# Optimization experiments

Measured on AMD Instinct MI355X. Metric: run time of the kernel, lower is better.

The kernel has to match this reference:

```python
import jax, jax.numpy as jnp
import numpy as np

DIM = 1024
HEADS = 16
DIM_HEAD = 64
INNER = HEADS * DIM_HEAD  # 1024


def setup_inputs() -> dict:
    key = jax.random.key(0)
    ks = jax.random.split(key, 5)
    B, N = 4, 2048
    x = jax.random.normal(ks[0], (B, N, DIM), dtype=jnp.float32)
    # nn.Linear weights stored as [out, in]; we keep [in, out] for x @ W
    s = 1.0 / np.sqrt(DIM)
    Wq = jax.random.uniform(ks[1], (DIM, INNER), jnp.float32, -s, s)
    Wkv = jax.random.uniform(ks[2], (DIM, 2 * INNER), jnp.float32, -s, s)
    so = 1.0 / np.sqrt(INNER)
    Wo = jax.random.uniform(ks[3], (INNER, DIM), jnp.float32, -so, so)
    bo = jax.random.uniform(ks[4], (DIM,), jnp.float32, -so, so)
    return {"x": x, "Wq": Wq, "Wkv": Wkv, "Wo": Wo, "bo": bo}


def reference(x, Wq, Wkv, Wo, bo):
    B, N, _ = x.shape
    scale = DIM_HEAD ** -0.5
    q = x @ Wq                      # [B, N, INNER]
    kv = x @ Wkv                    # [B, N, 2*INNER]
    k, v = jnp.split(kv, 2, axis=-1)

    def split_heads(t):
        return t.reshape(B, N, HEADS, DIM_HEAD).transpose(0, 2, 1, 3)  # b h n d

    q, k, v = map(split_heads, (q, k, v))
    dots = jnp.einsum('bhid,bhjd->bhij', q, k) * scale
    # causal mask: positions j > i filled with -inf
    causal = jnp.triu(jnp.ones((N, N), dtype=bool), k=1)
    dots = jnp.where(causal, -jnp.inf, dots)
    attn = jax.nn.softmax(dots, axis=-1)
    out = jnp.einsum('bhij,bhjd->bhid', attn, v)
    out = out.transpose(0, 2, 1, 3).reshape(B, N, INNER)
    return out @ Wo + bo
```

## Files before the change

kernel.cpp:

```cpp
#include <hip/hip_runtime.h>
#include <hip/hip_bf16.h>
#include <math.h>

typedef __attribute__((ext_vector_type(8))) short bf16x8;
typedef __attribute__((ext_vector_type(4))) float f32x4;

static __device__ inline ushort f2bf(float f) {
    union { float f; unsigned u; } v; v.f = f;
    unsigned r = (v.u + 0x7fff + ((v.u >> 16) & 1)) >> 16;
    return (ushort)r;
}

#define GLD_LDS(g, l) \
    __builtin_amdgcn_global_load_lds( \
        (const __attribute__((address_space(1))) void*)(g), \
        (__attribute__((address_space(3))) void*)(l), 16, 0, 0)

__global__ __launch_bounds__(256) void convert_x(
    const float* __restrict__ x, ushort* __restrict__ xb)
{
    const size_t i = ((size_t)blockIdx.x * 256 + threadIdx.x) * 8;
    float4 a = *(const float4*)(x + i);
    float4 b = *(const float4*)(x + i + 4);
    bf16x8 t;
    t[0] = (short)f2bf(a.x); t[1] = (short)f2bf(a.y);
    t[2] = (short)f2bf(a.z); t[3] = (short)f2bf(a.w);
    t[4] = (short)f2bf(b.x); t[5] = (short)f2bf(b.y);
    t[6] = (short)f2bf(b.z); t[7] = (short)f2bf(b.w);
    *(bf16x8*)(xb + i) = t;
}

__global__ __launch_bounds__(256) void prep_w(
    const float* __restrict__ Wq, const float* __restrict__ Wkv,
    const float* __restrict__ Wo, ushort* __restrict__ Wt)
{
    const int w = threadIdx.x >> 6;
    const int lane = threadIdx.x & 63;
    const int tile = blockIdx.x * 4 + w;
    const int r0 = (tile >> 4) << 6;
    const int k0 = (tile & 15) << 6;

    const float* src; int ld, c0;
    if (r0 < 1024)      { src = Wq;  ld = 1024; c0 = r0; }
    else if (r0 < 3072) { src = Wkv; ld = 2048; c0 = r0 - 1024; }
    else                { src = Wo;  ld = 1024; c0 = r0 - 3072; }

    ushort v[64];
    #pragma unroll
    for (int k = 0; k < 64; ++k)
        v[k] = f2bf(src[(size_t)(k0 + k) * ld + c0 + lane]);

    ushort* dst = Wt + (size_t)(r0 + lane) * 1024 + k0;
    #pragma unroll
    for (int k = 0; k < 64; k += 8) {
        bf16x8 t;
        #pragma unroll
        for (int j = 0; j < 8; ++j) t[j] = (short)v[k + j];
        *(bf16x8*)(dst + k) = t;
    }
}

#define STG32(t, Ad, Bd) { \
    GLD_LDS(aS + (size_t)(t) * 32, (Ad) + ldst); \
    GLD_LDS(bSlo + (size_t)(t) * 32, (Bd) + ldst); \
    GLD_LDS(bShi + (size_t)(t) * 32, (Bd) + 128 * 32 + ldst); }

#define GEMM_PIPE(Aptr, Btptr, NXT, NWG)                                       \
    __shared__ ushort As[3][128 * 32];                                         \
    __shared__ ushort Bs[3][256 * 32];                                         \
    const int tid = threadIdx.x;                                               \
    const int lane = tid & 63;                                                 \
    const int w = tid >> 6;                                                    \
    const int l15 = lane & 15;                                                 \
    const int quad = lane >> 4;                                                \
    const int wm = w >> 2, wn = w & 3;                                         \
    const int lin = blockIdx.y * (NXT) + blockIdx.x;                           \
    const int wg = (lin & 7) * ((NWG) >> 3) + (lin >> 3);                      \
    const int rowBase = (wg / (NXT)) * 128;                                    \
    const int colBase = (wg % (NXT)) * 256;                                    \
                         \
    const int sr = tid >> 2, sc = tid & 3;                                     \
    const int ldst = sr * 32 + sc * 8;                                         \
    const int gsw = (sc ^ ((sr >> 1) & 3)) << 3;                               \
    const ushort* aS   = (Aptr)  + (size_t)(rowBase + sr) * 1024 + gsw;        \
    const ushort* bSlo = (Btptr) + (size_t)(colBase + sr) * 1024 + gsw;        \
    const ushort* bShi = bSlo + (size_t)128 * 1024;                            \
    \
    const int co = ((quad ^ ((l15 >> 1) & 3)) << 3);                           \
    f32x4 acc[4][4];                                                           \
    _Pragma("unroll")                                                          \
    for (int i_ = 0; i_ < 4; ++i_)                                             \
        _Pragma("unroll")                                                      \
        for (int j_ = 0; j_ < 4; ++j_) acc[i_][j_] = (f32x4){0.f, 0.f, 0.f, 0.f}; \
    ushort *Acur = As[0], *Anxt = As[1], *Apre = As[2];                        \
    ushort *Bcur = Bs[0], *Bnxt = Bs[1], *Bpre = Bs[2];                        \
    STG32(0, Acur, Bcur)                                                       \
    STG32(1, Anxt, Bnxt)                                                       \
    asm volatile("s_waitcnt vmcnt(3)" ::: "memory");                           \
    __builtin_amdgcn_s_barrier();                                              \
    asm volatile("" ::: "memory");                                             \
    _Pragma("unroll 1")                                                        \
    for (int u = 0; u < 32; ++u) {                                             \
        if (u + 2 < 32) { STG32(u + 2, Apre, Bpre) }                           \
        const ushort* aC = Acur + (wm * 64 + l15) * 32;                        \
        const ushort* bC = Bcur + (wn * 64 + l15) * 32;                        \
        bf16x8 aF[4], bF[4];                                                   \
        _Pragma("unroll")                                                      \
        for (int ni = 0; ni < 4; ++ni)                                         \
            bF[ni] = *(const bf16x8*)(bC + ni * 512 + co);                     \
        _Pragma("unroll")                                                      \
        for (int mi = 0; mi < 4; ++mi)                                         \
            aF[mi] = *(const bf16x8*)(aC + mi * 512 + co);                     \
        __builtin_amdgcn_s_setprio(1);                                         \
        _Pragma("unroll")                                                      \
        for (int mi = 0; mi < 4; ++mi)                                         \
            _Pragma("unroll")                                                  \
            for (int ni = 0; ni < 4; ++ni)                                     \
                acc[mi][ni] = __builtin_amdgcn_mfma_f32_16x16x32_bf16(         \
                    aF[mi], bF[ni], acc[mi][ni], 0, 0, 0);                     \
        __builtin_amdgcn_s_setprio(0);                                         \
        if (u < 30)       { asm volatile("s_waitcnt vmcnt(3)" ::: "memory"); } \
        else if (u == 30) { asm volatile("s_waitcnt vmcnt(0)" ::: "memory"); } \
        if (u < 31) {                                                          \
            __builtin_amdgcn_s_barrier();                                      \
            asm volatile("" ::: "memory");                                     \
        }                                                                      \
        ushort* tA = Acur; Acur = Anxt; Anxt = Apre; Apre = tA;                \
        ushort* tB = Bcur; Bcur = Bnxt; Bnxt = Bpre; Bpre = tB;                \
    }

__global__ __launch_bounds__(512, 4) void gemm_qkv(
    const ushort* __restrict__ A, const ushort* __restrict__ Bt,
    ushort* __restrict__ Qb, ushort* __restrict__ Kb, ushort* __restrict__ Vt)
{
    GEMM_PIPE(A, Bt, 12, 768)

    const int seg = colBase >> 10;
    if (seg == 2) {
        #pragma unroll
        for (int mi = 0; mi < 4; ++mi) {
            #pragma unroll
            for (int ni = 0; ni < 4; ++ni) {
                const int c = (colBase + wn*64 + ni*16 + l15) & 1023;
                const int h = c >> 6, d = c & 63;
                const int m = rowBase + wm*64 + mi*16 + quad*4;
                const int b = m >> 11, nn = m & 2047;
                ushort4 v;
                v.x = f2bf(acc[mi][ni][0]); v.y = f2bf(acc[mi][ni][1]);
                v.z = f2bf(acc[mi][ni][2]); v.w = f2bf(acc[mi][ni][3]);
                *(ushort4*)(Vt + ((size_t)(b*16 + h)*64 + d)*2048 + nn) = v;
            }
        }
    } else {
        ushort* dst = seg ? Kb : Qb;
        const float sc2 = seg ? 1.0f : 0.18033688011112042f;
        #pragma unroll
        for (int mi = 0; mi < 4; ++mi) {
            #pragma unroll
            for (int ni = 0; ni < 4; ++ni) {
                const int c = (colBase + wn*64 + ni*16 + l15) & 1023;
                const int h = c >> 6, d = c & 63;
                #pragma unroll
                for (int r = 0; r < 4; ++r) {
                    const int m = rowBase + wm*64 + mi*16 + quad*4 + r;
                    const int b = m >> 11, nn = m & 2047;
                    dst[((((size_t)b*16 + h)*2048 + nn) << 6) + d] = f2bf(acc[mi][ni][r] * sc2);
                }
            }
        }
    }
}

__global__ __launch_bounds__(512, 4) void gemm_out(
    const ushort* __restrict__ A, const ushort* __restrict__ Bt,
    const float* __restrict__ bo, float* __restrict__ out)
{
    GEMM_PIPE(A, Bt, 4, 256)

    #pragma unroll
    for (int mi = 0; mi < 4; ++mi) {
        #pragma unroll
        for (int ni = 0; ni < 4; ++ni) {
            const int n = colBase + wn*64 + ni*16 + l15;
            const float bb = bo[n];
            #pragma unroll
            for (int r = 0; r < 4; ++r) {
                const int m = rowBase + wm*64 + mi*16 + quad*4 + r;
                out[(size_t)m * 1024 + n] = acc[mi][ni][r] + bb;
            }
        }
    }
}

__device__ __forceinline__ bf16x8 lds_frag(const ushort* S, int row, int chunk) {
    return *(const bf16x8*)(S + row * 64 + ((chunk ^ (row & 7)) << 3));
}

__global__ __launch_bounds__(256, 2) void flash_mfma(
    const ushort* __restrict__ Qb,
    const ushort* __restrict__ Kb,
    const ushort* __restrict__ Vt,
    ushort* __restrict__ Ob)
{
    __shared__ ushort Ks[2][4096];
    __shared__ ushort Vs[2][4096];
    __shared__ ushort PsAll[4][32][72];

    const int tid = threadIdx.x;
    const int w = tid >> 6;
    const int lane = tid & 63;
    const int l15 = lane & 15;
    const int quad = lane >> 4;
    ushort (*Ps)[72] = PsAll[w];

    const int blk = blockIdx.x;
    const int bh = ((blk & 7) << 3) | ((blk >> 3) & 7);
    const int qt = 15 - (blk >> 6);
    const int nt = 2 * qt + 2;
    const int rb0 = (qt << 7) + w * 32;

    const int sr0 = tid >> 3, sr1 = sr0 + 32;
    const int cg0 = (tid & 7) ^ (sr0 & 7);
    const int cg1 = (tid & 7) ^ (sr1 & 7);
    const ushort* kgb = Kb + (size_t)bh * 131072;
    const ushort* vgb = Vt + (size_t)bh * 131072;

    bf16x8 qf[2][2];
    #pragma unroll
    for (int mi = 0; mi < 2; ++mi) {
        const ushort* qp = Qb + ((size_t)bh * 2048 + rb0 + mi*16 + l15) * 64 + quad * 8;
        qf[mi][0] = *(const bf16x8*)qp;
        qf[mi][1] = *(const bf16x8*)(qp + 32);
    }

    bf16x8 bones;
    #pragma unroll
    for (int j = 0; j < 8; ++j) bones[j] = (short)0x3F80;

    float m_r[2];
    f32x4 o[2][4], lacc[2];
    #pragma unroll
    for (int mi = 0; mi < 2; ++mi) {
        m_r[mi] = -INFINITY;
        lacc[mi] = (f32x4){0.f, 0.f, 0.f, 0.f};
        #pragma unroll
        for (int nb = 0; nb < 4; ++nb) o[mi][nb] = (f32x4){0.f, 0.f, 0.f, 0.f};
    }

    GLD_LDS(kgb + sr0*64 + cg0*8, &Ks[0][tid*8]);
    GLD_LDS(kgb + sr1*64 + cg1*8, &Ks[0][tid*8 + 2048]);
    GLD_LDS(vgb + (size_t)sr0*2048 + cg0*8, &Vs[0][tid*8]);
    GLD_LDS(vgb + (size_t)sr1*2048 + cg1*8, &Vs[0][tid*8 + 2048]);

    for (int t = 0; t < nt; ++t) {
        __syncthreads();
        const int cur = t & 1;
        if (t + 1 < nt) {
            const int jn = t + 1;
            ushort* kd = &Ks[cur ^ 1][tid * 8];
            ushort* vd = &Vs[cur ^ 1][tid * 8];
            GLD_LDS(kgb + (size_t)jn*4096 + sr0*64 + cg0*8, kd);
            GLD_LDS(kgb + (size_t)jn*4096 + sr1*64 + cg1*8, kd + 2048);
            GLD_LDS(vgb + (size_t)sr0*2048 + jn*64 + cg0*8, vd);
            GLD_LDS(vgb + (size_t)sr1*2048 + jn*64 + cg1*8, vd + 2048);
        }
        const int j0 = t << 6;
        if (j0 > rb0 + 31) continue;

        const ushort* Ksb = Ks[cur];
        const ushort* Vsb = Vs[cur];

        f32x4 St[2][4];
        #pragma unroll
        for (int kb = 0; kb < 4; ++kb) {
            bf16x8 ka = lds_frag(Ksb, kb*16 + l15, quad);
            bf16x8 kc = lds_frag(Ksb, kb*16 + l15, quad + 4);
            #pragma unroll
            for (int mi = 0; mi < 2; ++mi) {
                f32x4 s = (f32x4){0.f, 0.f, 0.f, 0.f};
                s = __builtin_amdgcn_mfma_f32_16x16x32_bf16(ka, qf[mi][0], s, 0, 0, 0);
                s = __builtin_amdgcn_mfma_f32_16x16x32_bf16(kc, qf[mi][1], s, 0, 0, 0);
                St[mi][kb] = s;
            }
        }

        #pragma unroll
        for (int mi = 0; mi < 2; ++mi) {
            const int qrow = rb0 + mi*16 + l15;
            if (j0 + 63 > rb0 + mi*16) {
                #pragma unroll
                for (int kb = 0; kb < 4; ++kb) {
                    const int kbase = j0 + kb*16 + quad*4;
                    #pragma unroll
                    for (int r = 0; r < 4; ++r)
                        if (kbase + r > qrow) St[mi][kb][r] = -INFINITY;
                }
            }
            f32x4 mv = St[mi][0];
            #pragma unroll
            for (int kb = 1; kb < 4; ++kb)
                #pragma unroll
                for (int r = 0; r < 4; ++r) mv[r] = fmaxf(mv[r], St[mi][kb][r]);
            float mx = fmaxf(fmaxf(mv[0], mv[1]), fmaxf(mv[2], mv[3]));
            mx = fmaxf(mx, __shfl_xor(mx, 16));
            mx = fmaxf(mx, __shfl_xor(mx, 32));
            const float mold = m_r[mi];
            const float mnew = fmaxf(mold, mx);
            if (__any(mnew > mold)) {
                m_r[mi] = mnew;
                const float corr = __builtin_amdgcn_exp2f(mold - mnew);
                float ct[4];
                #pragma unroll
                for (int r = 0; r < 4; ++r) ct[r] = __shfl(corr, quad*4 + r);
                #pragma unroll
                for (int r = 0; r < 4; ++r) lacc[mi][r] *= ct[r];
                #pragma unroll
                for (int nb = 0; nb < 4; ++nb)
                    #pragma unroll
                    for (int r = 0; r < 4; ++r) o[mi][nb][r] *= ct[r];
            }
            #pragma unroll
            for (int kb = 0; kb < 4; ++kb)
                #pragma unroll
                for (int r = 0; r < 4; ++r)
                    St[mi][kb][r] = __builtin_amdgcn_exp2f(St[mi][kb][r] - mnew);
            #pragma unroll
            for (int kb = 0; kb < 4; ++kb) {
                union { float f; unsigned u; } c0, c1, c2, c3;
                c0.f = St[mi][kb][0]; c1.f = St[mi][kb][1];
                c2.f = St[mi][kb][2]; c3.f = St[mi][kb][3];
                uint2 pk;
                pk.x = (c0.u >> 16) | (c1.u & 0xFFFF0000u);
                pk.y = (c2.u >> 16) | (c3.u & 0xFFFF0000u);
                *(uint2*)&Ps[mi*16 + l15][kb*16 + quad*4] = pk;
            }
        }

        bf16x8 pf[2][2];
        #pragma unroll
        for (int mi = 0; mi < 2; ++mi) {
            pf[mi][0] = *(const bf16x8*)&Ps[mi*16 + l15][quad * 8];
            pf[mi][1] = *(const bf16x8*)&Ps[mi*16 + l15][32 + quad * 8];
        }
        #pragma unroll
        for (int mi = 0; mi < 2; ++mi) {
            lacc[mi] = __builtin_amdgcn_mfma_f32_16x16x32_bf16(pf[mi][0], bones, lacc[mi], 0, 0, 0);
            lacc[mi] = __builtin_amdgcn_mfma_f32_16x16x32_bf16(pf[mi][1], bones, lacc[mi], 0, 0, 0);
        }
        #pragma unroll
        for (int nb = 0; nb < 4; ++nb) {
            bf16x8 va = lds_frag(Vsb, nb*16 + l15, quad);
            bf16x8 vc = lds_frag(Vsb, nb*16 + l15, quad + 4);
            #pragma unroll
            for (int mi = 0; mi < 2; ++mi) {
                o[mi][nb] = __builtin_amdgcn_mfma_f32_16x16x32_bf16(pf[mi][0], va, o[mi][nb], 0, 0, 0);
                o[mi][nb] = __builtin_amdgcn_mfma_f32_16x16x32_bf16(pf[mi][1], vc, o[mi][nb], 0, 0, 0);
            }
        }
    }

    const int b = bh >> 4, h = bh & 15;
    #pragma unroll
    for (int mi = 0; mi < 2; ++mi)
        #pragma unroll
        for (int r = 0; r < 4; ++r) {
            const int ig = rb0 + mi*16 + quad*4 + r;
            const float inv = 1.f / lacc[mi][r];
            ushort* op = Ob + ((size_t)(b * 2048 + ig)) * 1024 + h * 64 + l15;
            #pragma unroll
            for (int nb = 0; nb < 4; ++nb)
                op[nb * 16] = f2bf(o[mi][nb][r] * inv);
        }
}

extern "C" void kernel_launch(void* const* d_in, const int* in_sizes, int n_in,
                              void* d_out, int out_size, void* d_ws, size_t ws_size,
                              hipStream_t stream) {
    const float* x   = (const float*)d_in[0];
    const float* Wq  = (const float*)d_in[1];
    const float* Wkv = (const float*)d_in[2];
    const float* Wo  = (const float*)d_in[3];
    const float* bo  = (const float*)d_in[4];
    float* out = (float*)d_out;

    const size_t SEG = (size_t)8388608 * 2;
    char* ws = (char*)d_ws;
    ushort* xb = (ushort*)(ws);
    ushort* Qb = (ushort*)(ws + SEG);
    ushort* Kb = (ushort*)(ws + SEG * 2);
    ushort* Vt = (ushort*)(ws + SEG * 3);
    ushort* Ob = (ushort*)(ws + SEG * 4);
    ushort* Wt = (ushort*)(ws + SEG * 5);

    convert_x<<<dim3(4096), 256, 0, stream>>>(x, xb);
    prep_w<<<dim3(256), 256, 0, stream>>>(Wq, Wkv, Wo, Wt);
    gemm_qkv<<<dim3(12, 64), 512, 0, stream>>>(xb, Wt, Qb, Kb, Vt);
    flash_mfma<<<dim3(1024), 256, 0, stream>>>(Qb, Kb, Vt, Ob);
    gemm_out<<<dim3(4, 64), 512, 0, stream>>>(Ob, Wt + (size_t)3072 * 1024, bo, out);
}
```

Measured before the change: 259.1 us.

## Rewrite QKV GEMM with 256x256 tiles and K=64 double-buffered staged pipeline

```diff
diff --git a/kernel.cpp b/kernel.cpp
--- a/kernel.cpp
+++ b/kernel.cpp
@@ -15,6 +15,8 @@
     __builtin_amdgcn_global_load_lds( \
         (const __attribute__((address_space(1))) void*)(g), \
         (__attribute__((address_space(3))) void*)(l), 16, 0, 0)
+
+#define MFMA_BF16(a, b, c) __builtin_amdgcn_mfma_f32_16x16x32_bf16((a), (b), (c), 0, 0, 0)
 
 __global__ __launch_bounds__(256) void convert_x(
     const float* __restrict__ x, ushort* __restrict__ xb)
@@ -57,6 +59,200 @@
         #pragma unroll
         for (int j = 0; j < 8; ++j) t[j] = (short)v[k + j];
         *(bf16x8*)(dst + k) = t;
+    }
+}
+
+#define STG_A256(t, h) { \
+    ushort* d_ = As2 + ((t) & 1) * 16384 + (h) * 8192 + tid * 8; \
+    GLD_LDS(aG + (size_t)((h) * 128) * 1024 + (size_t)(t) * 64, d_); \
+    GLD_LDS(aG + (size_t)((h) * 128 + 64) * 1024 + (size_t)(t) * 64, d_ + 4096); }
+#define STG_B256(t, h) { \
+    ushort* d_ = Bs2 + ((t) & 1) * 16384 + (h) * 8192 + tid * 8; \
+    GLD_LDS(bG + (size_t)((h) * 128) * 1024 + (size_t)(t) * 64, d_); \
+    GLD_LDS(bG + (size_t)((h) * 128 + 64) * 1024 + (size_t)(t) * 64, d_ + 4096); }
+
+__global__ __launch_bounds__(512, 2) void gemm_qkv(
+    const ushort* __restrict__ A, const ushort* __restrict__ Bt,
+    ushort* __restrict__ Qb, ushort* __restrict__ Kb, ushort* __restrict__ Vt)
+{
+    __shared__ ushort As2[2 * 2 * 8192];
+    __shared__ ushort Bs2[2 * 2 * 8192];
+
+    const int tid = threadIdx.x;
+    const int lane = tid & 63;
+    const int w = tid >> 6;
+    const int l15 = lane & 15;
+    const int quad = lane >> 4;
+    const int wm = w >> 2, wn = w & 3;
+
+    const int lin = blockIdx.y * 12 + blockIdx.x;
+    const int wg = (lin & 7) * 48 + (lin >> 3);
+    const int rowBase = (wg / 12) * 256;
+    const int colBase = (wg % 12) * 256;
+
+    const int srow = tid >> 3;
+    const int gsw = ((tid & 7) ^ (srow & 7)) << 3;
+    const ushort* aG = A  + (size_t)(rowBase + srow) * 1024 + gsw;
+    const ushort* bG = Bt + (size_t)(colBase + srow) * 1024 + gsw;
+
+    const int c0 = (quad ^ (l15 & 7)) << 3;
+    const int c1 = c0 ^ 32;
+
+    f32x4 acc[8][4];
+    #pragma unroll
+    for (int i_ = 0; i_ < 8; ++i_)
+        #pragma unroll
+        for (int j_ = 0; j_ < 4; ++j_) acc[i_][j_] = (f32x4){0.f, 0.f, 0.f, 0.f};
+
+    STG_A256(0, 0) STG_A256(0, 1) STG_B256(0, 0) STG_B256(0, 1)
+    asm volatile("s_waitcnt vmcnt(4)" ::: "memory");
+    STG_B256(1, 0) STG_A256(1, 0) STG_A256(1, 1)
+    asm volatile("s_waitcnt vmcnt(6)" ::: "memory");
+    __builtin_amdgcn_s_barrier();
+    asm volatile("" ::: "memory");
+
+    #pragma unroll 1
+    for (int t = 0; t < 16; ++t) {
+        const int cur = t & 1;
+        const ushort* Ar = As2 + cur * 16384;
+        const ushort* Br = Bs2 + cur * 16384;
+        const ushort* a0p = Ar + (wm * 64 + l15) * 64;
+        const ushort* a1p = a0p + 8192;
+        const ushort* bp  = Br + (wn >> 1) * 8192 + ((wn & 1) * 64 + l15) * 64;
+
+        bf16x8 b0[4], b1[4];
+        #pragma unroll
+        for (int ni = 0; ni < 4; ++ni) {
+            b0[ni] = *(const bf16x8*)(bp + ni * 1024 + c0);
+            b1[ni] = *(const bf16x8*)(bp + ni * 1024 + c1);
+        }
+        bf16x8 aE0 = *(const bf16x8*)(a0p + c0);
+        bf16x8 aO0 = *(const bf16x8*)(a0p + c1);
+        bf16x8 aE1 = *(const bf16x8*)(a0p + 1024 + c0);
+        bf16x8 aO1 = *(const bf16x8*)(a0p + 1024 + c1);
+        if (t + 1 < 16) { STG_B256(t + 1, 1) }
+        __builtin_amdgcn_s_barrier();
+        asm volatile("s_waitcnt lgkmcnt(0)" ::: "memory");
+        __builtin_amdgcn_sched_barrier(0);
+        __builtin_amdgcn_s_setprio(1);
+        #pragma unroll
+        for (int ni = 0; ni < 4; ++ni) {
+            acc[0][ni] = MFMA_BF16(aE0, b0[ni], acc[0][ni]);
+            acc[0][ni] = MFMA_BF16(aO0, b1[ni], acc[0][ni]);
+        }
+        #pragma unroll
+        for (int ni = 0; ni < 4; ++ni) {
+            acc[1][ni] = MFMA_BF16(aE1, b0[ni], acc[1][ni]);
+            acc[1][ni] = MFMA_BF16(aO1, b1[ni], acc[1][ni]);
+        }
+        __builtin_amdgcn_s_setprio(0);
+        __builtin_amdgcn_s_barrier();
+        asm volatile("" ::: "memory");
+
+        bf16x8 aE2 = *(const bf16x8*)(a0p + 2048 + c0);
+        bf16x8 aO2 = *(const bf16x8*)(a0p + 2048 + c1);
+        bf16x8 aE3 = *(const bf16x8*)(a0p + 3072 + c0);
+        bf16x8 aO3 = *(const bf16x8*)(a0p + 3072 + c1);
+        if (t + 2 < 16) { STG_B256(t + 2, 0) }
+        __builtin_amdgcn_s_barrier();
+        asm volatile("s_waitcnt lgkmcnt(0)" ::: "memory");
+        __builtin_amdgcn_sched_barrier(0);
+        __builtin_amdgcn_s_setprio(1);
+        #pragma unroll
+        for (int ni = 0; ni < 4; ++ni) {
+            acc[2][ni] = MFMA_BF16(aE2, b0[ni], acc[2][ni]);
+            acc[2][ni] = MFMA_BF16(aO2, b1[ni], acc[2][ni]);
+        }
+        #pragma unroll
+        for (int ni = 0; ni < 4; ++ni) {
+            acc[3][ni] = MFMA_BF16(aE3, b0[ni], acc[3][ni]);
+            acc[3][ni] = MFMA_BF16(aO3, b1[ni], acc[3][ni]);
+        }
+        __builtin_amdgcn_s_setprio(0);
+        __builtin_amdgcn_s_barrier();
+        asm volatile("" ::: "memory");
+
+        bf16x8 s1E[4], s1O[4];
+        #pragma unroll
+        for (int rf = 0; rf < 4; ++rf) {
+            s1E[rf] = *(const bf16x8*)(a1p + rf * 1024 + c0);
+            s1O[rf] = *(const bf16x8*)(a1p + rf * 1024 + c1);
+        }
+        if (t + 2 < 16) { STG_A256(t + 2, 0) }
+        __builtin_amdgcn_s_barrier();
+        asm volatile("s_waitcnt lgkmcnt(0)" ::: "memory");
+        __builtin_amdgcn_sched_barrier(0);
+        __builtin_amdgcn_s_setprio(1);
+        #pragma unroll
+        for (int ni = 0; ni < 4; ++ni) {
+            acc[4][ni] = MFMA_BF16(s1E[0], b0[ni], acc[4][ni]);
+            acc[4][ni] = MFMA_BF16(s1O[0], b1[ni], acc[4][ni]);
+        }
+        #pragma unroll
+        for (int ni = 0; ni < 4; ++ni) {
+            acc[5][ni] = MFMA_BF16(s1E[1], b0[ni], acc[5][ni]);
+            acc[5][ni] = MFMA_BF16(s1O[1], b1[ni], acc[5][ni]);
+        }
+        __builtin_amdgcn_s_setprio(0);
+        __builtin_amdgcn_s_barrier();
+        asm volatile("" ::: "memory");
+
+        if (t + 2 < 16) { STG_A256(t + 2, 1) }
+        __builtin_amdgcn_s_barrier();
+        __builtin_amdgcn_sched_barrier(0);
+        __builtin_amdgcn_s_setprio(1);
+        #pragma unroll
+        for (int ni = 0; ni < 4; ++ni) {
+            acc[6][ni] = MFMA_BF16(s1E[2], b0[ni], acc[6][ni]);
+            acc[6][ni] = MFMA_BF16(s1O[2], b1[ni], acc[6][ni]);
+        }
+        #pragma unroll
+        for (int ni = 0; ni < 4; ++ni) {
+            acc[7][ni] = MFMA_BF16(s1E[3], b0[ni], acc[7][ni]);
+            acc[7][ni] = MFMA_BF16(s1O[3], b1[ni], acc[7][ni]);
+        }
+        __builtin_amdgcn_s_setprio(0);
+        if (t < 14)       { asm volatile("s_waitcnt vmcnt(6)" ::: "memory"); }
+        else if (t == 14) { asm volatile("s_waitcnt vmcnt(0)" ::: "memory"); }
+        if (t < 15) {
+            __builtin_amdgcn_s_barrier();
+            asm volatile("" ::: "memory");
+        }
+    }
+
+    const int seg = colBase >> 10;
+    if (seg == 2) {
+        #pragma unroll
+        for (int ri = 0; ri < 8; ++ri) {
+            #pragma unroll
+            for (int ni = 0; ni < 4; ++ni) {
+                const int c = (colBase + wn*64 + ni*16 + l15) & 1023;
+                const int h = c >> 6, d = c & 63;
+                const int m = rowBase + ((ri >> 2) << 7) + wm*64 + (ri & 3)*16 + quad*4;
+                const int b = m >> 11, nn = m & 2047;
+                ushort4 v;
+                v.x = f2bf(acc[ri][ni][0]); v.y = f2bf(acc[ri][ni][1]);
+                v.z = f2bf(acc[ri][ni][2]); v.w = f2bf(acc[ri][ni][3]);
+                *(ushort4*)(Vt + ((size_t)(b*16 + h)*64 + d)*2048 + nn) = v;
+            }
+        }
+    } else {
+        ushort* dst = seg ? Kb : Qb;
+        const float sc2 = seg ? 1.0f : 0.18033688011112042f;
+        #pragma unroll
+        for (int ri = 0; ri < 8; ++ri) {
+            #pragma unroll
+            for (int ni = 0; ni < 4; ++ni) {
+                const int c = (colBase + wn*64 + ni*16 + l15) & 1023;
+                const int h = c >> 6, d = c & 63;
+                #pragma unroll
+                for (int r = 0; r < 4; ++r) {
+                    const int m = rowBase + ((ri >> 2) << 7) + wm*64 + (ri & 3)*16 + quad*4 + r;
+                    const int b = m >> 11, nn = m & 2047;
+                    dst[((((size_t)b*16 + h)*2048 + nn) << 6) + d] = f2bf(acc[ri][ni][r] * sc2);
+                }
+            }
+        }
     }
 }
 
@@ -78,14 +274,12 @@
     const int wg = (lin & 7) * ((NWG) >> 3) + (lin >> 3);                      \
     const int rowBase = (wg / (NXT)) * 128;                                    \
     const int colBase = (wg % (NXT)) * 256;                                    \
-                         \
     const int sr = tid >> 2, sc = tid & 3;                                     \
     const int ldst = sr * 32 + sc * 8;                                         \
     const int gsw = (sc ^ ((sr >> 1) & 3)) << 3;                               \
     const ushort* aS   = (Aptr)  + (size_t)(rowBase + sr) * 1024 + gsw;        \
     const ushort* bSlo = (Btptr) + (size_t)(colBase + sr) * 1024 + gsw;        \
     const ushort* bShi = bSlo + (size_t)128 * 1024;                            \
-    \
     const int co = ((quad ^ ((l15 >> 1) & 3)) << 3);                           \
     f32x4 acc[4][4];                                                           \
     _Pragma("unroll")                                                          \
@@ -129,48 +323,6 @@
         ushort* tB = Bcur; Bcur = Bnxt; Bnxt = Bpre; Bpre = tB;                \
     }
 
-__global__ __launch_bounds__(512, 4) void gemm_qkv(
-    const ushort* __restrict__ A, const ushort* __restrict__ Bt,
-    ushort* __restrict__ Qb, ushort* __restrict__ Kb, ushort* __restrict__ Vt)
-{
-    GEMM_PIPE(A, Bt, 12, 768)
-
-    const int seg = colBase >> 10;
-    if (seg == 2) {
-        #pragma unroll
-        for (int mi = 0; mi < 4; ++mi) {
-            #pragma unroll
-            for (int ni = 0; ni < 4; ++ni) {
-                const int c = (colBase + wn*64 + ni*16 + l15) & 1023;
-                const int h = c >> 6, d = c & 63;
-                const int m = rowBase + wm*64 + mi*16 + quad*4;
-                const int b = m >> 11, nn = m & 2047;
-                ushort4 v;
-                v.x = f2bf(acc[mi][ni][0]); v.y = f2bf(acc[mi][ni][1]);
-                v.z = f2bf(acc[mi][ni][2]); v.w = f2bf(acc[mi][ni][3]);
-                *(ushort4*)(Vt + ((size_t)(b*16 + h)*64 + d)*2048 + nn) = v;
-            }
-        }
-    } else {
-        ushort* dst = seg ? Kb : Qb;
-        const float sc2 = seg ? 1.0f : 0.18033688011112042f;
-        #pragma unroll
-        for (int mi = 0; mi < 4; ++mi) {
-            #pragma unroll
-            for (int ni = 0; ni < 4; ++ni) {
-                const int c = (colBase + wn*64 + ni*16 + l15) & 1023;
-                const int h = c >> 6, d = c & 63;
-                #pragma unroll
-                for (int r = 0; r < 4; ++r) {
-                    const int m = rowBase + wm*64 + mi*16 + quad*4 + r;
-                    const int b = m >> 11, nn = m & 2047;
-                    dst[((((size_t)b*16 + h)*2048 + nn) << 6) + d] = f2bf(acc[mi][ni][r] * sc2);
-                }
-            }
-        }
-    }
-}
-
 __global__ __launch_bounds__(512, 4) void gemm_out(
     const ushort* __restrict__ A, const ushort* __restrict__ Bt,
     const float* __restrict__ bo, float* __restrict__ out)
@@ -278,8 +430,8 @@
             #pragma unroll
             for (int mi = 0; mi < 2; ++mi) {
                 f32x4 s = (f32x4){0.f, 0.f, 0.f, 0.f};
-                s = __builtin_amdgcn_mfma_f32_16x16x32_bf16(ka, qf[mi][0], s, 0, 0, 0);
-                s = __builtin_amdgcn_mfma_f32_16x16x32_bf16(kc, qf[mi][1], s, 0, 0, 0);
+                s = MFMA_BF16(ka, qf[mi][0], s);
+                s = MFMA_BF16(kc, qf[mi][1], s);
                 St[mi][kb] = s;
             }
         }
@@ -326,12 +478,12 @@
                     St[mi][kb][r] = __builtin_amdgcn_exp2f(St[mi][kb][r] - mnew);
             #pragma unroll
             for (int kb = 0; kb < 4; ++kb) {
-                union { float f; unsigned u; } c0, c1, c2, c3;
-                c0.f = St[mi][kb][0]; c1.f = St[mi][kb][1];
-                c2.f = St[mi][kb][2]; c3.f = St[mi][kb][3];
+                union { float f; unsigned u; } c0_, c1_, c2_, c3_;
+                c0_.f = St[mi][kb][0]; c1_.f = St[mi][kb][1];
+                c2_.f = St[mi][kb][2]; c3_.f = St[mi][kb][3];
                 uint2 pk;
-                pk.x = (c0.u >> 16) | (c1.u & 0xFFFF0000u);
-                pk.y = (c2.u >> 16) | (c3.u & 0xFFFF0000u);
+                pk.x = (c0_.u >> 16) | (c1_.u & 0xFFFF0000u);
+                pk.y = (c2_.u >> 16) | (c3_.u & 0xFFFF0000u);
                 *(uint2*)&Ps[mi*16 + l15][kb*16 + quad*4] = pk;
             }
         }
@@ -344,8 +496,8 @@
         }
         #pragma unroll
         for (int mi = 0; mi < 2; ++mi) {
-            lacc[mi] = __builtin_amdgcn_mfma_f32_16x16x32_bf16(pf[mi][0], bones, lacc[mi], 0, 0, 0);
-            lacc[mi] = __builtin_amdgcn_mfma_f32_16x16x32_bf16(pf[mi][1], bones, lacc[mi], 0, 0, 0);
+            lacc[mi] = MFMA_BF16(pf[mi][0], bones, lacc[mi]);
+            lacc[mi] = MFMA_BF16(pf[mi][1], bones, lacc[mi]);
         }
         #pragma unroll
         for (int nb = 0; nb < 4; ++nb) {
@@ -353,8 +505,8 @@
             bf16x8 vc = lds_frag(Vsb, nb*16 + l15, quad + 4);
             #pragma unroll
             for (int mi = 0; mi < 2; ++mi) {
-                o[mi][nb] = __builtin_amdgcn_mfma_f32_16x16x32_bf16(pf[mi][0], va, o[mi][nb], 0, 0, 0);
-                o[mi][nb] = __builtin_amdgcn_mfma_f32_16x16x32_bf16(pf[mi][1], vc, o[mi][nb], 0, 0, 0);
+                o[mi][nb] = MFMA_BF16(pf[mi][0], va, o[mi][nb]);
+                o[mi][nb] = MFMA_BF16(pf[mi][1], vc, o[mi][nb]);
             }
         }
     }
@@ -394,7 +546,7 @@
 
     convert_x<<<dim3(4096), 256, 0, stream>>>(x, xb);
     prep_w<<<dim3(256), 256, 0, stream>>>(Wq, Wkv, Wo, Wt);
-    gemm_qkv<<<dim3(12, 64), 512, 0, stream>>>(xb, Wt, Qb, Kb, Vt);
+    gemm_qkv<<<dim3(12, 32), 512, 0, stream>>>(xb, Wt, Qb, Kb, Vt);
     flash_mfma<<<dim3(1024), 256, 0, stream>>>(Qb, Kb, Vt, Ob);
     gemm_out<<<dim3(4, 64), 512, 0, stream>>>(Ob, Wt + (size_t)3072 * 1024, bo, out);
 }
```

Result: no change. 258.1 us (-0.4%).

## Enlarge QKV GEMM tiles to 256x384 with double-buffered LDS staging

Applied to the files above, without the earlier changes.

```diff
diff --git a/kernel.cpp b/kernel.cpp
--- a/kernel.cpp
+++ b/kernel.cpp
@@ -15,6 +15,8 @@
     __builtin_amdgcn_global_load_lds( \
         (const __attribute__((address_space(1))) void*)(g), \
         (__attribute__((address_space(3))) void*)(l), 16, 0, 0)
+
+#define MFMA_BF16(a, b, c) __builtin_amdgcn_mfma_f32_16x16x32_bf16((a), (b), (c), 0, 0, 0)
 
 __global__ __launch_bounds__(256) void convert_x(
     const float* __restrict__ x, ushort* __restrict__ xb)
@@ -57,6 +59,109 @@
         #pragma unroll
         for (int j = 0; j < 8; ++j) t[j] = (short)v[k + j];
         *(bf16x8*)(dst + k) = t;
+    }
+}
+
+#define STG_A96(t) { ushort* d_ = As2 + ((t) & 1) * 8192 + ldst; \
+    GLD_LDS(aG + (size_t)(t) * 32, d_); \
+    GLD_LDS(aG + (size_t)131072 + (size_t)(t) * 32, d_ + 4096); }
+#define STG_B96(t) { ushort* d_ = Bs2 + ((t) & 1) * 12288 + ldst; \
+    GLD_LDS(bG + (size_t)(t) * 32, d_); \
+    GLD_LDS(bG + (size_t)131072 + (size_t)(t) * 32, d_ + 4096); \
+    GLD_LDS(bG + (size_t)262144 + (size_t)(t) * 32, d_ + 8192); }
+
+__global__ __launch_bounds__(512, 2) void gemm_qkv(
+    const ushort* __restrict__ A, const ushort* __restrict__ Bt,
+    ushort* __restrict__ Qb, ushort* __restrict__ Kb, ushort* __restrict__ Vt)
+{
+    __shared__ ushort As2[2 * 8192];
+    __shared__ ushort Bs2[2 * 12288];
+
+    const int tid = threadIdx.x;
+    const int lane = tid & 63;
+    const int w = tid >> 6;
+    const int l15 = lane & 15;
+    const int quad = lane >> 4;
+    const int wm = w >> 2, wn = w & 3;
+
+    const int lin = blockIdx.y * 8 + blockIdx.x;
+    const int wg = (lin & 7) * 32 + (lin >> 3);
+    const int rowBase = (wg >> 3) * 256;
+    const int colBase = (wg & 7) * 384;
+
+    const int sr = tid >> 2, sc = tid & 3;
+    const int ldst = sr * 32 + sc * 8;
+    const int gsw = (sc ^ ((sr >> 1) & 3)) << 3;
+    const ushort* aG = A  + (size_t)(rowBase + sr) * 1024 + gsw;
+    const ushort* bG = Bt + (size_t)(colBase + sr) * 1024 + gsw;
+
+    const int co = (quad ^ ((l15 >> 1) & 3)) << 3;
+
+    f32x4 acc[8][6];
+    #pragma unroll
+    for (int i_ = 0; i_ < 8; ++i_)
+        #pragma unroll
+        for (int j_ = 0; j_ < 6; ++j_) acc[i_][j_] = (f32x4){0.f, 0.f, 0.f, 0.f};
+
+    STG_A96(0) STG_B96(0)
+    asm volatile("s_waitcnt vmcnt(0)" ::: "memory");
+    __builtin_amdgcn_s_barrier();
+    asm volatile("" ::: "memory");
+
+    #pragma unroll 1
+    for (int t = 0; t < 32; ++t) {
+        const int cur = t & 1;
+        if (t + 1 < 32) { STG_A96(t + 1) STG_B96(t + 1) }
+
+        const ushort* aRd = As2 + cur * 8192  + (wm * 128 + l15) * 32;
+        const ushort* bRd = Bs2 + cur * 12288 + (wn * 96 + l15) * 32;
+
+        bf16x8 bF[6];
+        #pragma unroll
+        for (int ni = 0; ni < 6; ++ni)
+            bF[ni] = *(const bf16x8*)(bRd + ni * 512 + co);
+
+        __builtin_amdgcn_s_setprio(1);
+        #pragma unroll
+        for (int ri = 0; ri < 8; ++ri) {
+            bf16x8 aF = *(const bf16x8*)(aRd + ri * 512 + co);
+            #pragma unroll
+            for (int ni = 0; ni < 6; ++ni)
+                acc[ri][ni] = MFMA_BF16(aF, bF[ni], acc[ri][ni]);
+        }
+        __builtin_amdgcn_s_setprio(0);
+
+        asm volatile("s_waitcnt vmcnt(0)" ::: "memory");
+        __builtin_amdgcn_s_barrier();
+        asm volatile("" ::: "memory");
+    }
+
+    const float qsc = 0.18033688011112042f;
+    #pragma unroll
+    for (int ri = 0; ri < 8; ++ri) {
+        #pragma unroll
+        for (int ni = 0; ni < 6; ++ni) {
+            const int c = colBase + wn * 96 + ni * 16 + l15;
+            const int seg = c >> 10;
+            const int h = (c & 1023) >> 6, d = c & 63;
+            if (seg == 2) {
+                const int m = rowBase + wm * 128 + ri * 16 + quad * 4;
+                const int b = m >> 11, nn = m & 2047;
+                ushort4 v;
+                v.x = f2bf(acc[ri][ni][0]); v.y = f2bf(acc[ri][ni][1]);
+                v.z = f2bf(acc[ri][ni][2]); v.w = f2bf(acc[ri][ni][3]);
+                *(ushort4*)(Vt + ((size_t)(b * 16 + h) * 64 + d) * 2048 + nn) = v;
+            } else {
+                ushort* dst = seg ? Kb : Qb;
+                const float sc2 = seg ? 1.0f : qsc;
+                #pragma unroll
+                for (int r = 0; r < 4; ++r) {
+                    const int m = rowBase + wm * 128 + ri * 16 + quad * 4 + r;
+                    const int b = m >> 11, nn = m & 2047;
+                    dst[((((size_t)b * 16 + h) * 2048 + nn) << 6) + d] = f2bf(acc[ri][ni][r] * sc2);
+                }
+            }
+        }
     }
 }
 
@@ -78,14 +183,12 @@
     const int wg = (lin & 7) * ((NWG) >> 3) + (lin >> 3);                      \
     const int rowBase = (wg / (NXT)) * 128;                                    \
     const int colBase = (wg % (NXT)) * 256;                                    \
-                         \
     const int sr = tid >> 2, sc = tid & 3;                                     \
     const int ldst = sr * 32 + sc * 8;                                         \
     const int gsw = (sc ^ ((sr >> 1) & 3)) << 3;                               \
     const ushort* aS   = (Aptr)  + (size_t)(rowBase + sr) * 1024 + gsw;        \
     const ushort* bSlo = (Btptr) + (size_t)(colBase + sr) * 1024 + gsw;        \
     const ushort* bShi = bSlo + (size_t)128 * 1024;                            \
-    \
     const int co = ((quad ^ ((l15 >> 1) & 3)) << 3);                           \
     f32x4 acc[4][4];                                                           \
     _Pragma("unroll")                                                          \
@@ -129,48 +232,6 @@
         ushort* tB = Bcur; Bcur = Bnxt; Bnxt = Bpre; Bpre = tB;                \
     }
 
-__global__ __launch_bounds__(512, 4) void gemm_qkv(
-    const ushort* __restrict__ A, const ushort* __restrict__ Bt,
-    ushort* __restrict__ Qb, ushort* __restrict__ Kb, ushort* __restrict__ Vt)
-{
-    GEMM_PIPE(A, Bt, 12, 768)
-
-    const int seg = colBase >> 10;
-    if (seg == 2) {
-        #pragma unroll
-        for (int mi = 0; mi < 4; ++mi) {
-            #pragma unroll
-            for (int ni = 0; ni < 4; ++ni) {
-                const int c = (colBase + wn*64 + ni*16 + l15) & 1023;
-                const int h = c >> 6, d = c & 63;
-                const int m = rowBase + wm*64 + mi*16 + quad*4;
-                const int b = m >> 11, nn = m & 2047;
-                ushort4 v;
-                v.x = f2bf(acc[mi][ni][0]); v.y = f2bf(acc[mi][ni][1]);
-                v.z = f2bf(acc[mi][ni][2]); v.w = f2bf(acc[mi][ni][3]);
-                *(ushort4*)(Vt + ((size_t)(b*16 + h)*64 + d)*2048 + nn) = v;
-            }
-        }
-    } else {
-        ushort* dst = seg ? Kb : Qb;
-        const float sc2 = seg ? 1.0f : 0.18033688011112042f;
-        #pragma unroll
-        for (int mi = 0; mi < 4; ++mi) {
-            #pragma unroll
-            for (int ni = 0; ni < 4; ++ni) {
-                const int c = (colBase + wn*64 + ni*16 + l15) & 1023;
-                const int h = c >> 6, d = c & 63;
-                #pragma unroll
-                for (int r = 0; r < 4; ++r) {
-                    const int m = rowBase + wm*64 + mi*16 + quad*4 + r;
-                    const int b = m >> 11, nn = m & 2047;
-                    dst[((((size_t)b*16 + h)*2048 + nn) << 6) + d] = f2bf(acc[mi][ni][r] * sc2);
-                }
-            }
-        }
-    }
-}
-
 __global__ __launch_bounds__(512, 4) void gemm_out(
     const ushort* __restrict__ A, const ushort* __restrict__ Bt,
     const float* __restrict__ bo, float* __restrict__ out)
@@ -278,8 +339,8 @@
             #pragma unroll
             for (int mi = 0; mi < 2; ++mi) {
                 f32x4 s = (f32x4){0.f, 0.f, 0.f, 0.f};
-                s = __builtin_amdgcn_mfma_f32_16x16x32_bf16(ka, qf[mi][0], s, 0, 0, 0);
-                s = __builtin_amdgcn_mfma_f32_16x16x32_bf16(kc, qf[mi][1], s, 0, 0, 0);
+                s = MFMA_BF16(ka, qf[mi][0], s);
+                s = MFMA_BF16(kc, qf[mi][1], s);
                 St[mi][kb] = s;
             }
         }
@@ -326,12 +387,12 @@
                     St[mi][kb][r] = __builtin_amdgcn_exp2f(St[mi][kb][r] - mnew);
             #pragma unroll
             for (int kb = 0; kb < 4; ++kb) {
-                union { float f; unsigned u; } c0, c1, c2, c3;
-                c0.f = St[mi][kb][0]; c1.f = St[mi][kb][1];
-                c2.f = St[mi][kb][2]; c3.f = St[mi][kb][3];
+                union { float f; unsigned u; } c0_, c1_, c2_, c3_;
+                c0_.f = St[mi][kb][0]; c1_.f = St[mi][kb][1];
+                c2_.f = St[mi][kb][2]; c3_.f = St[mi][kb][3];
                 uint2 pk;
-                pk.x = (c0.u >> 16) | (c1.u & 0xFFFF0000u);
-                pk.y = (c2.u >> 16) | (c3.u & 0xFFFF0000u);
+                pk.x = (c0_.u >> 16) | (c1_.u & 0xFFFF0000u);
+                pk.y = (c2_.u >> 16) | (c3_.u & 0xFFFF0000u);
                 *(uint2*)&Ps[mi*16 + l15][kb*16 + quad*4] = pk;
             }
         }
@@ -344,8 +405,8 @@
         }
         #pragma unroll
         for (int mi = 0; mi < 2; ++mi) {
-            lacc[mi] = __builtin_amdgcn_mfma_f32_16x16x32_bf16(pf[mi][0], bones, lacc[mi], 0, 0, 0);
-            lacc[mi] = __builtin_amdgcn_mfma_f32_16x16x32_bf16(pf[mi][1], bones, lacc[mi], 0, 0, 0);
+            lacc[mi] = MFMA_BF16(pf[mi][0], bones, lacc[mi]);
+            lacc[mi] = MFMA_BF16(pf[mi][1], bones, lacc[mi]);
         }
         #pragma unroll
         for (int nb = 0; nb < 4; ++nb) {
@@ -353,8 +414,8 @@
             bf16x8 vc = lds_frag(Vsb, nb*16 + l15, quad + 4);
             #pragma unroll
             for (int mi = 0; mi < 2; ++mi) {
-                o[mi][nb] = __builtin_amdgcn_mfma_f32_16x16x32_bf16(pf[mi][0], va, o[mi][nb], 0, 0, 0);
-                o[mi][nb] = __builtin_amdgcn_mfma_f32_16x16x32_bf16(pf[mi][1], vc, o[mi][nb], 0, 0, 0);
+                o[mi][nb] = MFMA_BF16(pf[mi][0], va, o[mi][nb]);
+                o[mi][nb] = MFMA_BF16(pf[mi][1], vc, o[mi][nb]);
             }
         }
     }
@@ -394,7 +455,7 @@
 
     convert_x<<<dim3(4096), 256, 0, stream>>>(x, xb);
     prep_w<<<dim3(256), 256, 0, stream>>>(Wq, Wkv, Wo, Wt);
-    gemm_qkv<<<dim3(12, 64), 512, 0, stream>>>(xb, Wt, Qb, Kb, Vt);
+    gemm_qkv<<<dim3(8, 32), 512, 0, stream>>>(xb, Wt, Qb, Kb, Vt);
     flash_mfma<<<dim3(1024), 256, 0, stream>>>(Qb, Kb, Vt, Ob);
     gemm_out<<<dim3(4, 64), 512, 0, stream>>>(Ob, Wt + (size_t)3072 * 1024, bo, out);
 }
```

After: 253.5 us. 1.02x faster.
